# Kernel optimization log

Measured on AMD Instinct MI355X. Metric: run time of the kernel, lower is better.

Reference implementation:

```python
import jax, jax.numpy as jnp
import numpy as np

B, S, H, D = 2, 4096, 32, 128
R = 2            # num_reflectors
BASE = 10000.0   # rope base
EPS = 1e-6


def setup_inputs() -> dict:
    key = jax.random.key(0)
    k1, k2, k3 = jax.random.split(key, 3)
    q = jax.random.normal(k1, (B, S, H, D), jnp.float32)
    k = jax.random.normal(k2, (B, S, H, D), jnp.float32)
    pos = jnp.arange(S, dtype=jnp.float32)
    reflectors = jax.random.normal(k3, (H, R, D), jnp.float32)
    return {"q": q, "k": k, "pos": pos, "reflectors": reflectors}


def _apply_householder(x, reflectors, eps):
    # x: [B,S,H,D]; reflectors: [H,R,D]. Apply chain of per-head reflections
    # H = prod_r (I - 2 v_r v_r^T / (||v_r||^2 + eps)).
    n_refl = reflectors.shape[1]
    for r in range(n_refl):  # small fixed loop over reflectors
        v = reflectors[:, r, :]                      # [H,D]
        vf = v.astype(jnp.float32)
        sq = jnp.sum(vf * vf, axis=-1) + eps         # [H], fp32 accumulation
        dot = jnp.einsum('bshd,hd->bsh', x.astype(jnp.float32), vf)  # [B,S,H]
        coef = (2.0 * dot / sq).astype(x.dtype)      # [B,S,H]
        x = x - coef[..., None] * v                  # rank-1 update per head
    return x


def _rope(x, pos, base):
    # Block-diagonal 2x2 rotations on adjacent pairs (rope_ndim=2).
    d = x.shape[-1]
    d2 = d // 2
    inv_freq = base ** (-(jnp.arange(d2, dtype=jnp.float32) * 2.0) / d)  # [d2]
    ang = pos[:, None] * inv_freq                     # [S,d2]
    cos = jnp.cos(ang)[None, :, None, :]              # [1,S,1,d2]
    sin = jnp.sin(ang)[None, :, None, :]
    xr = x.reshape(*x.shape[:-1], d2, 2)              # [B,S,H,d2,2]
    x0, x1 = xr[..., 0], xr[..., 1]
    out = jnp.stack([x0 * cos - x1 * sin, x0 * sin + x1 * cos], axis=-1)
    return out.reshape(x.shape)


def reference(q, k, pos, reflectors):
    qh = _apply_householder(q, reflectors, EPS)
    kh = _apply_householder(k, reflectors, EPS)
    return _rope(qh, pos, BASE), _rope(kh, pos, BASE)
```

## Files before the change

### kernel.cpp

```cpp
#include <hip/hip_runtime.h>
#include <math.h>

#define BB 2
#define SS 4096
#define HH 32
#define DD 128
#define EPS_C 1e-6f
#define C_LOG (-0.20762050593046015f)

typedef float vf4 __attribute__((ext_vector_type(4)));

__device__ __forceinline__ float hsum32(float v) {
    v += __int_as_float(__builtin_amdgcn_ds_swizzle(__float_as_int(v), 0x041F));
    v += __int_as_float(__builtin_amdgcn_ds_swizzle(__float_as_int(v), 0x081F));
    v += __int_as_float(__builtin_amdgcn_ds_swizzle(__float_as_int(v), 0x101F));
    v += __int_as_float(__builtin_amdgcn_ds_swizzle(__float_as_int(v), 0x201F));
    v += __int_as_float(__builtin_amdgcn_ds_swizzle(__float_as_int(v), 0x401F));
    return v;
}

__device__ __forceinline__ float dot4(vf4 a, vf4 b) {
    return a.x * b.x + a.y * b.y + a.z * b.z + a.w * b.w;
}

__device__ __forceinline__ vf4 finish(vf4 x, vf4 v0, vf4 v1,
                                      float d0, float d1,
                                      float rs0, float rs1, float t01,
                                      float sa, float ca, float sb, float cb) {
    const float c0 = d0 * rs0;
    const float c1 = (d1 - c0 * t01) * rs1;
    x.x -= c0 * v0.x + c1 * v1.x;
    x.y -= c0 * v0.y + c1 * v1.y;
    x.z -= c0 * v0.z + c1 * v1.z;
    x.w -= c0 * v0.w + c1 * v1.w;
    vf4 r;
    r.x = x.x * ca - x.y * sa;  r.y = x.x * sa + x.y * ca;
    r.z = x.z * cb - x.w * sb;  r.w = x.z * sb + x.w * cb;
    return r;
}

__global__ __launch_bounds__(256, 6)
void hh_rope_kernel(const float* __restrict__ q, const float* __restrict__ k,
                    const float* __restrict__ pos, const float* __restrict__ refl,
                    float* __restrict__ oq, float* __restrict__ ok)
{
    const int lane   = threadIdx.x & 63;
    const int wid    = (blockIdx.x << 2) + (threadIdx.x >> 6);
    const int hp     = wid & 15;
    const int slice  = wid >> 4;
    const int half   = lane >> 5;
    const int j      = lane & 31;
    const int h      = (hp << 1) + half;

    const vf4 v0 = ((const vf4*)(refl + (size_t)(h * 2 + 0) * DD))[j];
    const vf4 v1 = ((const vf4*)(refl + (size_t)(h * 2 + 1) * DD))[j];
    const float rs0 = 2.0f / (hsum32(dot4(v0, v0)) + EPS_C);
    const float rs1 = 2.0f / (hsum32(dot4(v1, v1)) + EPS_C);
    const float t01 = hsum32(dot4(v1, v0));

    const float if0 = exp2f((float)(2 * j)     * C_LOG);
    const float if1 = exp2f((float)(2 * j + 1) * C_LOG);

    for (int bs = slice << 1; bs < BB * SS; bs += 1024) {
        const size_t row0 = ((size_t)bs * HH + h) * DD + 4 * (size_t)j;
        const size_t row1 = row0 + (size_t)HH * DD;

        vf4 xq0 = __builtin_nontemporal_load((const vf4*)(q + row0));
        vf4 xk0 = __builtin_nontemporal_load((const vf4*)(k + row0));
        vf4 xq1 = __builtin_nontemporal_load((const vf4*)(q + row1));
        vf4 xk1 = __builtin_nontemporal_load((const vf4*)(k + row1));

        const float p0 = pos[bs & (SS - 1)];
        const float p1 = pos[(bs + 1) & (SS - 1)];

        float sA0, cA0, sB0, cB0, sA1, cA1, sB1, cB1;
        __sincosf(p0 * if0, &sA0, &cA0);
        __sincosf(p0 * if1, &sB0, &cB0);
        __sincosf(p1 * if0, &sA1, &cA1);
        __sincosf(p1 * if1, &sB1, &cB1);

        const float dq00 = hsum32(dot4(xq0, v0));
        const float dq01 = hsum32(dot4(xq0, v1));
        const float dk00 = hsum32(dot4(xk0, v0));
        const float dk01 = hsum32(dot4(xk0, v1));
        const float dq10 = hsum32(dot4(xq1, v0));
        const float dq11 = hsum32(dot4(xq1, v1));
        const float dk10 = hsum32(dot4(xk1, v0));
        const float dk11 = hsum32(dot4(xk1, v1));

        vf4 r;
        r = finish(xq0, v0, v1, dq00, dq01, rs0, rs1, t01, sA0, cA0, sB0, cB0);
        __builtin_nontemporal_store(r, (vf4*)(oq + row0));
        r = finish(xk0, v0, v1, dk00, dk01, rs0, rs1, t01, sA0, cA0, sB0, cB0);
        __builtin_nontemporal_store(r, (vf4*)(ok + row0));
        r = finish(xq1, v0, v1, dq10, dq11, rs0, rs1, t01, sA1, cA1, sB1, cB1);
        __builtin_nontemporal_store(r, (vf4*)(oq + row1));
        r = finish(xk1, v0, v1, dk10, dk11, rs0, rs1, t01, sA1, cA1, sB1, cB1);
        __builtin_nontemporal_store(r, (vf4*)(ok + row1));
    }
}

extern "C" void kernel_launch(void* const* d_in, const int* in_sizes, int n_in,
                              void* d_out, int out_size, void* d_ws, size_t ws_size,
                              hipStream_t stream) {
    const float* q    = (const float*)d_in[0];
    const float* k    = (const float*)d_in[1];
    const float* pos  = (const float*)d_in[2];
    const float* refl = (const float*)d_in[3];

    float* oq = (float*)d_out;
    float* ok = oq + (size_t)BB * SS * HH * DD;

    hh_rope_kernel<<<dim3(2048), dim3(256), 0, stream>>>(q, k, pos, refl, oq, ok);
}
```

Baseline: 426.6 us.

## Software-pipeline row loads two iterations ahead with fully unrolled fixed loop

Replaces the strided loop, which handled two rows per iteration, with a fully unrolled 16-iteration loop over single rows. Loads for the row two steps ahead are issued before the current row is computed, keeping more memory requests in flight per wave. The trip count is hardcoded to match the grid and shape, and the unrolling plus the prefetch buffers raise register pressure under the 6-waves launch bound.

```diff
diff --git a/kernel.cpp b/kernel.cpp
--- a/kernel.cpp
+++ b/kernel.cpp
@@ -39,6 +39,11 @@
     return r;
 }
 
+__device__ __forceinline__ size_t it_off(int it) {
+    return (size_t)(it >> 1) * ((size_t)1024 * HH * DD)
+         + (size_t)(it & 1)  * ((size_t)HH * DD);
+}
+
 __global__ __launch_bounds__(256, 6)
 void hh_rope_kernel(const float* __restrict__ q, const float* __restrict__ k,
                     const float* __restrict__ pos, const float* __restrict__ refl,
@@ -61,42 +66,47 @@
     const float if0 = exp2f((float)(2 * j)     * C_LOG);
     const float if1 = exp2f((float)(2 * j + 1) * C_LOG);
 
-    for (int bs = slice << 1; bs < BB * SS; bs += 1024) {
-        const size_t row0 = ((size_t)bs * HH + h) * DD + 4 * (size_t)j;
-        const size_t row1 = row0 + (size_t)HH * DD;
+    const int bs0 = slice << 1;
+    const size_t base = ((size_t)bs0 * HH + h) * DD + 4 * (size_t)j;
+    const float* qp = q  + base;
+    const float* kp = k  + base;
+    float*      oqp = oq + base;
+    float*      okp = ok + base;
 
-        vf4 xq0 = __builtin_nontemporal_load((const vf4*)(q + row0));
-        vf4 xk0 = __builtin_nontemporal_load((const vf4*)(k + row0));
-        vf4 xq1 = __builtin_nontemporal_load((const vf4*)(q + row1));
-        vf4 xk1 = __builtin_nontemporal_load((const vf4*)(k + row1));
+    vf4 aq = __builtin_nontemporal_load((const vf4*)(qp + it_off(0)));
+    vf4 ak = __builtin_nontemporal_load((const vf4*)(kp + it_off(0)));
+    vf4 bq = __builtin_nontemporal_load((const vf4*)(qp + it_off(1)));
+    vf4 bk = __builtin_nontemporal_load((const vf4*)(kp + it_off(1)));
 
-        const float p0 = pos[bs & (SS - 1)];
-        const float p1 = pos[(bs + 1) & (SS - 1)];
+#pragma unroll
+    for (int it = 0; it < 16; ++it) {
+        vf4 cq, ck;
+        if (it < 14) {
+            const size_t poff = it_off(it + 2);
+            cq = __builtin_nontemporal_load((const vf4*)(qp + poff));
+            ck = __builtin_nontemporal_load((const vf4*)(kp + poff));
+        }
 
-        float sA0, cA0, sB0, cB0, sA1, cA1, sB1, cB1;
-        __sincosf(p0 * if0, &sA0, &cA0);
-        __sincosf(p0 * if1, &sB0, &cB0);
-        __sincosf(p1 * if0, &sA1, &cA1);
-        __sincosf(p1 * if1, &sB1, &cB1);
+        const int bs = bs0 + ((it >> 1) << 10) + (it & 1);
+        const float p = pos[bs & (SS - 1)];
+        float sa, ca, sb, cb;
+        __sincosf(p * if0, &sa, &ca);
+        __sincosf(p * if1, &sb, &cb);
 
-        const float dq00 = hsum32(dot4(xq0, v0));
-        const float dq01 = hsum32(dot4(xq0, v1));
-        const float dk00 = hsum32(dot4(xk0, v0));
-        const float dk01 = hsum32(dot4(xk0, v1));
-        const float dq10 = hsum32(dot4(xq1, v0));
-        const float dq11 = hsum32(dot4(xq1, v1));
-        const float dk10 = hsum32(dot4(xk1, v0));
-        const float dk11 = hsum32(dot4(xk1, v1));
+        const float dq0 = hsum32(dot4(aq, v0));
+        const float dq1 = hsum32(dot4(aq, v1));
+        const float dk0 = hsum32(dot4(ak, v0));
+        const float dk1 = hsum32(dot4(ak, v1));
 
+        const size_t off = it_off(it);
         vf4 r;
-        r = finish(xq0, v0, v1, dq00, dq01, rs0, rs1, t01, sA0, cA0, sB0, cB0);
-        __builtin_nontemporal_store(r, (vf4*)(oq + row0));
-        r = finish(xk0, v0, v1, dk00, dk01, rs0, rs1, t01, sA0, cA0, sB0, cB0);
-        __builtin_nontemporal_store(r, (vf4*)(ok + row0));
-        r = finish(xq1, v0, v1, dq10, dq11, rs0, rs1, t01, sA1, cA1, sB1, cB1);
-        __builtin_nontemporal_store(r, (vf4*)(oq + row1));
-        r = finish(xk1, v0, v1, dk10, dk11, rs0, rs1, t01, sA1, cA1, sB1, cB1);
-        __builtin_nontemporal_store(r, (vf4*)(ok + row1));
+        r = finish(aq, v0, v1, dq0, dq1, rs0, rs1, t01, sa, ca, sb, cb);
+        __builtin_nontemporal_store(r, (vf4*)(oqp + off));
+        r = finish(ak, v0, v1, dk0, dk1, rs0, rs1, t01, sa, ca, sb, cb);
+        __builtin_nontemporal_store(r, (vf4*)(okp + off));
+
+        aq = bq; ak = bk;
+        if (it < 14) { bq = cq; bk = ck; }
     }
 }
 
```

Measured after the change: 431.5 us. About the same (+1.1%).
